# Kernel optimization log

Hardware: AMD Instinct MI355X
Metric: run time of the kernel (lower is better)

Reference implementation:

```python
import jax, jax.numpy as jnp
import numpy as np

NUM_HEADS = 16
MASKED_BIAS = -10000.0


def setup_inputs() -> dict:
    key = jax.random.key(0)
    k1, k2, k3 = jax.random.split(key, 3)
    B, S, D = 4, 2048, 1024
    scale = 0.02
    return {
        "hidden_states": jax.random.normal(k1, (B, S, D), dtype=jnp.float32),
        "c_attn_w": jax.random.normal(k2, (D, 3 * D), dtype=jnp.float32) * scale,
        "c_attn_b": jnp.zeros((3 * D,), dtype=jnp.float32),
        "c_proj_w": jax.random.normal(k3, (D, D), dtype=jnp.float32) * scale,
        "c_proj_b": jnp.zeros((D,), dtype=jnp.float32),
    }


def reference(hidden_states, c_attn_w, c_attn_b, c_proj_w, c_proj_b):
    B, S, D = hidden_states.shape
    H = NUM_HEADS
    hd = D // H
    # qkv projection (HF Conv1D: x @ W + b)
    qkv = hidden_states @ c_attn_w + c_attn_b  # [B, S, 3D]
    q, k, v = jnp.split(qkv, 3, axis=-1)

    def split_heads(t):
        return t.reshape(B, S, H, hd).transpose(0, 2, 1, 3)  # [B, H, S, hd]

    q, k, v = split_heads(q), split_heads(k), split_heads(v)
    # full score matrix [B, H, S, S] (eager attention)
    attn = jnp.einsum("bhqd,bhkd->bhqk", q, k) / jnp.sqrt(jnp.float32(hd))
    causal = jnp.tril(jnp.ones((S, S), dtype=bool))  # [S, S]
    attn = jnp.where(causal[None, None], attn, jnp.float32(MASKED_BIAS))
    attn = jax.nn.softmax(attn, axis=-1)
    out = jnp.einsum("bhqk,bhkd->bhqd", attn, v)  # [B, H, S, hd]
    out = out.transpose(0, 2, 1, 3).reshape(B, S, D)  # merge heads
    out = out @ c_proj_w + c_proj_b
    return out
```

## Files before the change

### kernel.cpp

```cpp
#include <hip/hip_runtime.h>

#define NH 16
#define HD 64

typedef __attribute__((ext_vector_type(8))) _Float16 f16x8;
typedef __attribute__((ext_vector_type(4))) float f32x4;
typedef __attribute__((ext_vector_type(8))) unsigned short us8;
typedef __attribute__((ext_vector_type(4))) unsigned short us4;
typedef __attribute__((ext_vector_type(2))) unsigned int u32x2;

#define CEXP 0.18033688f

__device__ __forceinline__ unsigned short f2h(float f) {
    _Float16 h = (_Float16)f;
    return __builtin_bit_cast(unsigned short, h);
}

__global__ __launch_bounds__(256)
void transpose_cast(const float* __restrict__ in, unsigned short* __restrict__ out,
                    int R, int C) {
    __shared__ float T[64][65];
    const int c0 = blockIdx.x * 64, r0 = blockIdx.y * 64;
    const int tid = threadIdx.x;
    const int rr = tid >> 4, cc4 = (tid & 15) * 4;
    #pragma unroll
    for (int p = 0; p < 4; ++p) {
        int r = rr + p * 16;
        float4 v = *reinterpret_cast<const float4*>(
            in + (size_t)(r0 + r) * C + c0 + cc4);
        T[r][cc4] = v.x; T[r][cc4 + 1] = v.y; T[r][cc4 + 2] = v.z; T[r][cc4 + 3] = v.w;
    }
    __syncthreads();
    #pragma unroll
    for (int p = 0; p < 4; ++p) {
        int orow = rr + p * 16;
        us4 w;
        #pragma unroll
        for (int j = 0; j < 4; ++j) w[j] = f2h(T[cc4 + j][orow]);
        *reinterpret_cast<us4*>(out + (size_t)(c0 + orow) * R + r0 + cc4) = w;
    }
}

__device__ __forceinline__ void stage128(unsigned short* dst,
                                         const unsigned short* src, int stride) {
    const int tid = threadIdx.x;
    #pragma unroll
    for (int p = 0; p < 4; ++p) {
        int idx = tid + p * 256;
        int r = idx >> 3;
        int slot = idx & 7;
        us8 v = *reinterpret_cast<const us8*>(src + (size_t)r * stride + slot * 8);
        int cb = (slot << 4) ^ ((r & 7) << 4);
        *reinterpret_cast<us8*>(reinterpret_cast<char*>(dst) + r * 128 + cb) = v;
    }
}

__device__ __forceinline__ void stage128_f32(unsigned short* dst,
                                             const float* src, int stride) {
    const int tid = threadIdx.x;
    #pragma unroll
    for (int p = 0; p < 4; ++p) {
        int idx = tid + p * 256;
        int r = idx >> 3;
        int slot = idx & 7;
        const float* s = src + (size_t)r * stride + slot * 8;
        float4 a = *reinterpret_cast<const float4*>(s);
        float4 b = *reinterpret_cast<const float4*>(s + 4);
        uint4 w;
        w.x = __builtin_bit_cast(unsigned int, __builtin_amdgcn_cvt_pkrtz(a.x, a.y));
        w.y = __builtin_bit_cast(unsigned int, __builtin_amdgcn_cvt_pkrtz(a.z, a.w));
        w.z = __builtin_bit_cast(unsigned int, __builtin_amdgcn_cvt_pkrtz(b.x, b.y));
        w.w = __builtin_bit_cast(unsigned int, __builtin_amdgcn_cvt_pkrtz(b.z, b.w));
        int cb = (slot << 4) ^ ((r & 7) << 4);
        *reinterpret_cast<uint4*>(reinterpret_cast<char*>(dst) + r * 128 + cb) = w;
    }
}

__device__ __forceinline__ void stage64(unsigned short* dst,
                                        const unsigned short* src, int stride) {
    const int tid = threadIdx.x;
    #pragma unroll
    for (int p = 0; p < 2; ++p) {
        int idx = tid + p * 256;
        int r = idx >> 3;
        int slot = idx & 7;
        us8 v = *reinterpret_cast<const us8*>(src + (size_t)r * stride + slot * 8);
        int cb = (slot << 4) ^ ((r & 7) << 4);
        *reinterpret_cast<us8*>(reinterpret_cast<char*>(dst) + r * 128 + cb) = v;
    }
}

__device__ __forceinline__ f16x8 frag16(const unsigned short* base, int row0, int ks) {
    const int lane = threadIdx.x & 63;
    const int r = row0 + (lane & 15);
    int cb = ((ks << 6) + (lane & 48)) ^ ((r & 7) << 4);
    return *reinterpret_cast<const f16x8*>(
        reinterpret_cast<const char*>(base) + r * 128 + cb);
}

template<int MODE>
__global__ __launch_bounds__(256)
void gemm_f16(const void* __restrict__ Ax,
              const unsigned short* __restrict__ Bt,
              const float* __restrict__ bias,
              float* __restrict__ C,
              unsigned short* __restrict__ qb,
              unsigned short* __restrict__ kb,
              unsigned short* __restrict__ vtb,
              int M, int N, int K) {
    __shared__ __align__(16) unsigned short As[128 * 64];
    __shared__ __align__(16) unsigned short Bs[128 * 64];

    const int tid = threadIdx.x;
    const int wid = tid >> 6, lane = tid & 63, g = lane >> 4;
    const int wr = wid >> 1, wc = wid & 1;
    const int m0 = blockIdx.y * 128, n0 = blockIdx.x * 128;

    f32x4 acc[4][4];
    #pragma unroll
    for (int i = 0; i < 4; ++i)
        #pragma unroll
        for (int j = 0; j < 4; ++j) {
            acc[i][j][0] = 0.f; acc[i][j][1] = 0.f;
            acc[i][j][2] = 0.f; acc[i][j][3] = 0.f;
        }

    for (int k0 = 0; k0 < K; k0 += 64) {
        __syncthreads();
        if (MODE == 1)
            stage128_f32(As, (const float*)Ax + (size_t)m0 * K + k0, K);
        else
            stage128(As, (const unsigned short*)Ax + (size_t)m0 * K + k0, K);
        stage128(Bs, Bt + (size_t)n0 * K + k0, K);
        __syncthreads();

        f16x8 af[4][2], bf[4][2];
        #pragma unroll
        for (int mi = 0; mi < 4; ++mi)
            #pragma unroll
            for (int ks = 0; ks < 2; ++ks)
                af[mi][ks] = frag16(As, wr * 64 + mi * 16, ks);
        #pragma unroll
        for (int ni = 0; ni < 4; ++ni)
            #pragma unroll
            for (int ks = 0; ks < 2; ++ks)
                bf[ni][ks] = frag16(Bs, wc * 64 + ni * 16, ks);

        __builtin_amdgcn_s_setprio(1);
        #pragma unroll
        for (int ks = 0; ks < 2; ++ks)
            #pragma unroll
            for (int mi = 0; mi < 4; ++mi)
                #pragma unroll
                for (int ni = 0; ni < 4; ++ni)
                    acc[mi][ni] = __builtin_amdgcn_mfma_f32_16x16x32_f16(
                        af[mi][ks], bf[ni][ks], acc[mi][ni], 0, 0, 0);
        __builtin_amdgcn_s_setprio(0);
    }

    const int colBase = n0 + wc * 64;
    const int rowBase = m0 + wr * 64;

    if (MODE == 0) {
        #pragma unroll
        for (int ni = 0; ni < 4; ++ni) {
            int col = colBase + ni * 16 + (lane & 15);
            float bv = bias[col];
            #pragma unroll
            for (int mi = 0; mi < 4; ++mi) {
                int row = rowBase + mi * 16 + g * 4;
                #pragma unroll
                for (int reg = 0; reg < 4; ++reg)
                    C[(size_t)(row + reg) * N + col] = acc[mi][ni][reg] + bv;
            }
        }
    } else {
        #pragma unroll
        for (int ni = 0; ni < 4; ++ni) {
            int col = colBase + ni * 16 + (lane & 15);
            float bv = bias[col];
            int seg = col >> 10;
            int cc = col & 1023;
            int h = cc >> 6, d = cc & 63;
            const float sc = (seg == 0) ? CEXP : 1.0f;
            #pragma unroll
            for (int mi = 0; mi < 4; ++mi) {
                int row = rowBase + mi * 16 + g * 4;
                int b = row >> 11, s = row & 2047;
                size_t bh = (size_t)(b * NH + h);
                if (seg < 2) {
                    unsigned short* dst = (seg ? kb : qb)
                        + bh * 2048 * 64 + (size_t)s * 64 + d;
                    #pragma unroll
                    for (int reg = 0; reg < 4; ++reg)
                        dst[(size_t)reg * 64] = f2h((acc[mi][ni][reg] + bv) * sc);
                } else {
                    unsigned short* dst = vtb
                        + bh * 64 * 2048 + (size_t)d * 2048 + s;
                    us4 w;
                    #pragma unroll
                    for (int reg = 0; reg < 4; ++reg)
                        w[reg] = f2h(acc[mi][ni][reg] + bv);
                    *reinterpret_cast<us4*>(dst) = w;
                }
            }
        }
    }
}

template<bool DIAG>
__device__ __forceinline__ void attn_tile(
    f16x8 qf0, f16x8 qf1,
    const unsigned short* Ks, const unsigned short* Vs, unsigned short* Pw,
    f32x4 (&o)[4], float& l_,
    int kt, int qrow_base, int lane, int g) {

    f32x4 s[4];
    #pragma unroll
    for (int n = 0; n < 4; ++n) { s[n][0] = 0.f; s[n][1] = 0.f; s[n][2] = 0.f; s[n][3] = 0.f; }

    __builtin_amdgcn_s_setprio(1);
    #pragma unroll
    for (int ks = 0; ks < 2; ++ks) {
        f16x8 b = ks ? qf1 : qf0;
        #pragma unroll
        for (int n = 0; n < 4; ++n)
            s[n] = __builtin_amdgcn_mfma_f32_16x16x32_f16(
                frag16(Ks, n * 16, ks), b, s[n], 0, 0, 0);
    }
    __builtin_amdgcn_s_setprio(0);

    const int q = lane & 15;
    float psum = 0.f;
    #pragma unroll
    for (int n = 0; n < 4; ++n) {
        float p0 = __builtin_exp2f(s[n][0]);
        float p1 = __builtin_exp2f(s[n][1]);
        float p2 = __builtin_exp2f(s[n][2]);
        float p3 = __builtin_exp2f(s[n][3]);
        if (DIAG) {
            const int kb_ = kt * 64 + (g << 2) + 16 * n;
            const int qg = qrow_base + q;
            p0 = (kb_ + 0 > qg) ? 0.f : p0;
            p1 = (kb_ + 1 > qg) ? 0.f : p1;
            p2 = (kb_ + 2 > qg) ? 0.f : p2;
            p3 = (kb_ + 3 > qg) ? 0.f : p3;
        }
        psum += (p0 + p1) + (p2 + p3);
        u32x2 w;
        w[0] = __builtin_bit_cast(unsigned int, __builtin_amdgcn_cvt_pkrtz(p0, p1));
        w[1] = __builtin_bit_cast(unsigned int, __builtin_amdgcn_cvt_pkrtz(p2, p3));
        int pcb = ((n << 5) + (g << 3)) ^ ((q & 7) << 4);
        *reinterpret_cast<u32x2*>(
            reinterpret_cast<char*>(Pw) + q * 128 + pcb) = w;
    }
    l_ += psum;

    __builtin_amdgcn_s_setprio(1);
    #pragma unroll
    for (int ks = 0; ks < 2; ++ks) {
        f16x8 pa = frag16(Pw, 0, ks);
        #pragma unroll
        for (int n = 0; n < 4; ++n)
            o[n] = __builtin_amdgcn_mfma_f32_16x16x32_f16(
                pa, frag16(Vs, n * 16, ks), o[n], 0, 0, 0);
    }
    __builtin_amdgcn_s_setprio(0);
}

__global__ __launch_bounds__(256, 4)
void attn_mfma(const unsigned short* __restrict__ qb,
               const unsigned short* __restrict__ kb,
               const unsigned short* __restrict__ vtb,
               unsigned short* __restrict__ attno) {
    const int f = blockIdx.x;
    const int xcd = f & 7;
    const int wi = f >> 3;
    const int bh = xcd * 8 + (wi >> 4);
    const int pair = wi & 15;
    const int qtA = pair, qtB = 31 - pair;
    const int tid = threadIdx.x;
    const int wid = tid >> 6, lane = tid & 63, g = lane >> 4;

    __shared__ __align__(16) unsigned short Ks[64 * 64];
    __shared__ __align__(16) unsigned short Vs[64 * 64];
    __shared__ __align__(16) unsigned short Ps[4][16 * 64];

    const unsigned short* kg0 = kb + (size_t)bh * 2048 * 64;
    const unsigned short* vg0 = vtb + (size_t)bh * 64 * 2048;

    const int qrl = wid * 16 + (lane & 15);
    const int qd0 = (lane >> 4) * 8;
    const unsigned short* qbase = qb + (size_t)bh * 2048 * 64;
    f16x8 qA0 = *reinterpret_cast<const f16x8*>(qbase + (size_t)(qtA * 64 + qrl) * 64 + qd0);
    f16x8 qA1 = *reinterpret_cast<const f16x8*>(qbase + (size_t)(qtA * 64 + qrl) * 64 + 32 + qd0);
    f16x8 qB0 = *reinterpret_cast<const f16x8*>(qbase + (size_t)(qtB * 64 + qrl) * 64 + qd0);
    f16x8 qB1 = *reinterpret_cast<const f16x8*>(qbase + (size_t)(qtB * 64 + qrl) * 64 + 32 + qd0);

    f32x4 oA[4], oB[4];
    float lA = 0.f, lB = 0.f;
    #pragma unroll
    for (int n = 0; n < 4; ++n) {
        #pragma unroll
        for (int r = 0; r < 4; ++r) { oA[n][r] = 0.f; oB[n][r] = 0.f; }
    }

    unsigned short* Pw = Ps[wid];
    const int qrbA = qtA * 64 + wid * 16;
    const int qrbB = qtB * 64 + wid * 16;

    auto STAGE = [&](int kt) {
        __syncthreads();
        stage64(Ks, kg0 + (size_t)kt * 64 * 64, 64);
        stage64(Vs, vg0 + (size_t)kt * 64, 2048);
        __syncthreads();
    };

    for (int kt = 0; kt < qtA; ++kt) {
        STAGE(kt);
        attn_tile<false>(qB0, qB1, Ks, Vs, Pw, oB, lB, kt, qrbB, lane, g);
        attn_tile<false>(qA0, qA1, Ks, Vs, Pw, oA, lA, kt, qrbA, lane, g);
    }
    STAGE(qtA);
    attn_tile<false>(qB0, qB1, Ks, Vs, Pw, oB, lB, qtA, qrbB, lane, g);
    attn_tile<true >(qA0, qA1, Ks, Vs, Pw, oA, lA, qtA, qrbA, lane, g);
    for (int kt = qtA + 1; kt < qtB; ++kt) {
        STAGE(kt);
        attn_tile<false>(qB0, qB1, Ks, Vs, Pw, oB, lB, kt, qrbB, lane, g);
    }
    STAGE(qtB);
    attn_tile<true >(qB0, qB1, Ks, Vs, Pw, oB, lB, qtB, qrbB, lane, g);

    const int b = bh >> 4, h = bh & 15;
    #pragma unroll
    for (int ph = 0; ph < 2; ++ph) {
        const int qt = ph ? qtB : qtA;
        f32x4* o = ph ? oB : oA;
        float ltot = ph ? lB : lA;
        ltot += __shfl_xor(ltot, 16);
        ltot += __shfl_xor(ltot, 32);
        unsigned short* ob = attno
            + (size_t)(b * 2048 + qt * 64 + wid * 16) * 1024 + h * 64;
        #pragma unroll
        for (int reg = 0; reg < 4; ++reg) {
            int row = (g << 2) + reg;
            float inv = 1.0f / __shfl(ltot, row);
            #pragma unroll
            for (int n = 0; n < 4; ++n)
                ob[(size_t)row * 1024 + n * 16 + (lane & 15)] = f2h(o[n][reg] * inv);
        }
    }
}

extern "C" void kernel_launch(void* const* d_in, const int* in_sizes, int n_in,
                              void* d_out, int out_size, void* d_ws, size_t ws_size,
                              hipStream_t stream) {
    const float* x    = (const float*)d_in[0];
    const float* Wqkv = (const float*)d_in[1];
    const float* bqkv = (const float*)d_in[2];
    const float* Wp   = (const float*)d_in[3];
    const float* bp   = (const float*)d_in[4];
    float* out = (float*)d_out;

    const int B = 4, S = 2048, D = 1024;
    const int M = B * S;
    const size_t HSZ = (size_t)M * D;

    unsigned short* wqt   = (unsigned short*)d_ws;
    unsigned short* wpt   = wqt + (size_t)3 * D * D;
    unsigned short* qbuf  = wpt + (size_t)D * D;
    unsigned short* kbuf  = qbuf + HSZ;
    unsigned short* vtb   = kbuf + HSZ;
    unsigned short* attno = vtb + HSZ;

    dim3 blk(256);
    transpose_cast<<<dim3(3 * D / 64, D / 64), blk, 0, stream>>>(Wqkv, wqt, D, 3 * D);
    transpose_cast<<<dim3(D / 64, D / 64), blk, 0, stream>>>(Wp, wpt, D, D);

    gemm_f16<1><<<dim3(3 * D / 128, M / 128), blk, 0, stream>>>(
        x, wqt, bqkv, nullptr, qbuf, kbuf, vtb, M, 3 * D, D);
    attn_mfma<<<dim3(1024), blk, 0, stream>>>(qbuf, kbuf, vtb, attno);
    gemm_f16<0><<<dim3(D / 128, M / 128), blk, 0, stream>>>(
        attno, wpt, bp, out, nullptr, nullptr, nullptr, M, D, D);
}
```

Before: 179.4 us.

## Swizzle GEMM block order and transpose MFMA operands for vectorized Q/K stores

Both GEMMs now use a 1D grid with grouped block ordering, where groups of 8 row-tiles sweep the columns, to improve L2 reuse of the A and B tiles. For the Q and K segments of the QKV GEMM, the MFMA operands are swapped so each lane holds 4 consecutive head-dim values. This lets the epilogue write packed 8-byte fp16 stores instead of strided scalar 2-byte stores. The cost is an extra branch, a vectorized bias load, and more epilogue code paths.

```diff
diff --git a/kernel.cpp b/kernel.cpp
--- a/kernel.cpp
+++ b/kernel.cpp
@@ -107,14 +107,20 @@
               unsigned short* __restrict__ qb,
               unsigned short* __restrict__ kb,
               unsigned short* __restrict__ vtb,
-              int M, int N, int K) {
+              int M, int N, int K, int nx) {
     __shared__ __align__(16) unsigned short As[128 * 64];
     __shared__ __align__(16) unsigned short Bs[128 * 64];
 
     const int tid = threadIdx.x;
     const int wid = tid >> 6, lane = tid & 63, g = lane >> 4;
     const int wr = wid >> 1, wc = wid & 1;
-    const int m0 = blockIdx.y * 128, n0 = blockIdx.x * 128;
+
+    const int f = blockIdx.x;
+    const int wi = f >> 3;
+    const int m0 = ((wi / nx) * 8 + (f & 7)) * 128;
+    const int n0 = (wi % nx) * 128;
+
+    const bool SWAPT = (MODE == 1) && (n0 < 2048);
 
     f32x4 acc[4][4];
     #pragma unroll
@@ -147,14 +153,25 @@
                 bf[ni][ks] = frag16(Bs, wc * 64 + ni * 16, ks);
 
         __builtin_amdgcn_s_setprio(1);
-        #pragma unroll
-        for (int ks = 0; ks < 2; ++ks)
-            #pragma unroll
-            for (int mi = 0; mi < 4; ++mi)
+        if (SWAPT) {
+            #pragma unroll
+            for (int ks = 0; ks < 2; ++ks)
                 #pragma unroll
-                for (int ni = 0; ni < 4; ++ni)
-                    acc[mi][ni] = __builtin_amdgcn_mfma_f32_16x16x32_f16(
-                        af[mi][ks], bf[ni][ks], acc[mi][ni], 0, 0, 0);
+                for (int mi = 0; mi < 4; ++mi)
+                    #pragma unroll
+                    for (int ni = 0; ni < 4; ++ni)
+                        acc[mi][ni] = __builtin_amdgcn_mfma_f32_16x16x32_f16(
+                            bf[ni][ks], af[mi][ks], acc[mi][ni], 0, 0, 0);
+        } else {
+            #pragma unroll
+            for (int ks = 0; ks < 2; ++ks)
+                #pragma unroll
+                for (int mi = 0; mi < 4; ++mi)
+                    #pragma unroll
+                    for (int ni = 0; ni < 4; ++ni)
+                        acc[mi][ni] = __builtin_amdgcn_mfma_f32_16x16x32_f16(
+                            af[mi][ks], bf[ni][ks], acc[mi][ni], 0, 0, 0);
+        }
         __builtin_amdgcn_s_setprio(0);
     }
 
@@ -174,35 +191,47 @@
                     C[(size_t)(row + reg) * N + col] = acc[mi][ni][reg] + bv;
             }
         }
+    } else if (SWAPT) {
+        unsigned short* qk = (n0 < 1024) ? qb : kb;
+        const float sc = (n0 < 1024) ? CEXP : 1.0f;
+        #pragma unroll
+        for (int ni = 0; ni < 4; ++ni) {
+            int nbase = colBase + ni * 16 + (g << 2);
+            float4 bv4 = *reinterpret_cast<const float4*>(bias + nbase);
+            const float* bvp = reinterpret_cast<const float*>(&bv4);
+            int cc = nbase & 1023;
+            int h = cc >> 6, d0 = cc & 63;
+            #pragma unroll
+            for (int mi = 0; mi < 4; ++mi) {
+                int m_idx = rowBase + mi * 16 + (lane & 15);
+                int b = m_idx >> 11, s = m_idx & 2047;
+                unsigned short* dst = qk
+                    + ((size_t)(b * NH + h) * 2048 + s) * 64 + d0;
+                us4 w;
+                #pragma unroll
+                for (int reg = 0; reg < 4; ++reg)
+                    w[reg] = f2h((acc[mi][ni][reg] + bvp[reg]) * sc);
+                *reinterpret_cast<us4*>(dst) = w;
+            }
+        }
     } else {
         #pragma unroll
         for (int ni = 0; ni < 4; ++ni) {
             int col = colBase + ni * 16 + (lane & 15);
             float bv = bias[col];
-            int seg = col >> 10;
             int cc = col & 1023;
             int h = cc >> 6, d = cc & 63;
-            const float sc = (seg == 0) ? CEXP : 1.0f;
             #pragma unroll
             for (int mi = 0; mi < 4; ++mi) {
                 int row = rowBase + mi * 16 + g * 4;
                 int b = row >> 11, s = row & 2047;
-                size_t bh = (size_t)(b * NH + h);
-                if (seg < 2) {
-                    unsigned short* dst = (seg ? kb : qb)
-                        + bh * 2048 * 64 + (size_t)s * 64 + d;
-                    #pragma unroll
-                    for (int reg = 0; reg < 4; ++reg)
-                        dst[(size_t)reg * 64] = f2h((acc[mi][ni][reg] + bv) * sc);
-                } else {
-                    unsigned short* dst = vtb
-                        + bh * 64 * 2048 + (size_t)d * 2048 + s;
-                    us4 w;
-                    #pragma unroll
-                    for (int reg = 0; reg < 4; ++reg)
-                        w[reg] = f2h(acc[mi][ni][reg] + bv);
-                    *reinterpret_cast<us4*>(dst) = w;
-                }
+                unsigned short* dst = vtb
+                    + (size_t)(b * NH + h) * 64 * 2048 + (size_t)d * 2048 + s;
+                us4 w;
+                #pragma unroll
+                for (int reg = 0; reg < 4; ++reg)
+                    w[reg] = f2h(acc[mi][ni][reg] + bv);
+                *reinterpret_cast<us4*>(dst) = w;
             }
         }
     }
@@ -377,9 +406,9 @@
     transpose_cast<<<dim3(3 * D / 64, D / 64), blk, 0, stream>>>(Wqkv, wqt, D, 3 * D);
     transpose_cast<<<dim3(D / 64, D / 64), blk, 0, stream>>>(Wp, wpt, D, D);
 
-    gemm_f16<1><<<dim3(3 * D / 128, M / 128), blk, 0, stream>>>(
-        x, wqt, bqkv, nullptr, qbuf, kbuf, vtb, M, 3 * D, D);
+    gemm_f16<1><<<dim3(1536), blk, 0, stream>>>(
+        x, wqt, bqkv, nullptr, qbuf, kbuf, vtb, M, 3 * D, D, 24);
     attn_mfma<<<dim3(1024), blk, 0, stream>>>(qbuf, kbuf, vtb, attno);
-    gemm_f16<0><<<dim3(D / 128, M / 128), blk, 0, stream>>>(
-        attno, wpt, bp, out, nullptr, nullptr, nullptr, M, D, D);
-}
+    gemm_f16<0><<<dim3(512), blk, 0, stream>>>(
+        attno, wpt, bp, out, nullptr, nullptr, nullptr, M, D, D, 8);
+}
```

New measurement: 192.9 us. +7.5%, slower.
